# Optimization experiments

Measured on AMD Instinct MI355X. Metric: run time of the kernel, lower is better.

Reference implementation:

```python
import jax, jax.numpy as jnp
import numpy as np

NEG_SLOPE = 0.2


def setup_inputs() -> dict:
    key = jax.random.key(0)
    k1, k2, k3, k4, k5 = jax.random.split(key, 5)
    N, F_in, F_out, H, D = 4096, 256, 256, 4, 64
    x = jax.random.normal(k1, (N, F_in), dtype=jnp.float32)
    adj = jax.random.normal(k2, (N, N), dtype=jnp.float32)  # ~half entries > 0 -> edges
    W = jax.random.normal(k3, (F_out, F_in), dtype=jnp.float32) * (1.0 / np.sqrt(F_in))
    a_src = jax.random.normal(k4, (H, D), dtype=jnp.float32) * 0.1
    a_dst = jax.random.normal(k5, (H, D), dtype=jnp.float32) * 0.1
    return {"x": x, "adj": adj, "W": W, "a_src": a_src, "a_dst": a_dst}


def reference(x, adj, W, a_src, a_dst):
    N = x.shape[0]
    H, D = a_src.shape
    # linear projection (torch Linear: x @ W.T), reshape to heads
    h = (x @ W.T).reshape(N, H, D)                      # [N, H, D]
    attn_src = jnp.einsum('nhd,hd->nh', h, a_src)       # [N, H]
    attn_dst = jnp.einsum('nhd,hd->nh', h, a_dst)       # [N, H]
    scores = attn_src[:, None, :] + attn_dst[None, :, :]  # [N, N, H]
    scores = jnp.where(scores >= 0, scores, NEG_SLOPE * scores)  # leaky_relu(0.2)
    mask = (adj > 0)[:, :, None]                        # [N, N, 1]
    scores = jnp.where(mask, scores, -jnp.inf)
    attn = jax.nn.softmax(scores, axis=1)               # softmax over neighbors j
    attn = jnp.nan_to_num(attn, nan=0.0)                # fully-masked rows -> 0
    weighted = attn * adj[:, :, None]                   # weight by adjacency values
    out = jnp.einsum('ijh,jhd->ihd', weighted, h)       # [N, H, D]
    return out.reshape(N, H * D)
```

## Files before the change

### kernel.cpp

```cpp
#include <hip/hip_runtime.h>
#include <stdint.h>

#define NN 4096
#define FF 256
#define HH 4
#define DD 64
#define NEG 0.2f
#define LOG2E 1.4426950408889634f

#define ITILE 32
#define CJ 64
#define NB (NN / 8)

typedef __attribute__((ext_vector_type(8))) short short8;
typedef __attribute__((ext_vector_type(4))) float f32x4;
typedef __attribute__((ext_vector_type(16))) float f32x16;

__device__ __forceinline__ uint16_t bf16_rh(float f) {
    uint32_t u = __float_as_uint(f);
    return (uint16_t)((u + 0x8000u) >> 16);
}
__device__ __forceinline__ uint32_t cvtpk(float lo, float hi) {
    uint32_t r;
    asm("v_cvt_pk_bf16_f32 %0, %1, %2" : "=v"(r) : "v"(lo), "v"(hi));
    return r;
}

__global__ __launch_bounds__(256) void gemm_h(const float* __restrict__ x,
                                              const float* __restrict__ W,
                                              const float* __restrict__ a_src,
                                              const float* __restrict__ a_dst,
                                              float* __restrict__ s,
                                              float* __restrict__ T_T,
                                              uint16_t* __restrict__ Bf,
                                              float* __restrict__ pden) {
    __shared__ uint16_t xs[64][264];
    __shared__ uint16_t wsl[64][264];
    const int tid = threadIdx.x;
    if (blockIdx.y == 0) pden[blockIdx.x * 256 + tid] = 0.f;
    const int i0g = blockIdx.x * 64;
    const int f0 = blockIdx.y * 64;
    const int hh = blockIdx.y;
    const float* xsrc = x + (size_t)i0g * FF;
    const float* wsrc = W + (size_t)f0 * FF;
    {
        const int rw = tid >> 6, c4 = (tid & 63) * 4;
#pragma unroll
        for (int p = 0; p < 16; p++) {
            float4 vx = ((const float4*)xsrc)[p * 256 + tid];
            float4 vw = ((const float4*)wsrc)[p * 256 + tid];
            *(uint2*)&xs[p * 4 + rw][c4] =
                make_uint2(cvtpk(vx.x, vx.y), cvtpk(vx.z, vx.w));
            *(uint2*)&wsl[p * 4 + rw][c4] =
                make_uint2(cvtpk(vw.x, vw.y), cvtpk(vw.z, vw.w));
        }
    }
    __syncthreads();
    const int w = tid >> 6, l = tid & 63;
    const int m = l & 15, q = l >> 4;
    const int i0 = i0g + w * 16;
    f32x4 acc[4];
#pragma unroll
    for (int n = 0; n < 4; n++)
#pragma unroll
        for (int r = 0; r < 4; r++) acc[n][r] = 0.f;
    const uint16_t* ax = &xs[w * 16 + m][q * 8];
#pragma unroll
    for (int k0 = 0; k0 < 8; k0++) {
        short8 af = *(const short8*)(ax + k0 * 32);
#pragma unroll
        for (int n = 0; n < 4; n++) {
            short8 bf = *(const short8*)&wsl[n * 16 + m][k0 * 32 + q * 8];
            acc[n] = __builtin_amdgcn_mfma_f32_16x16x32_bf16(af, bf, acc[n], 0, 0, 0);
        }
    }
    const float* as = a_src + hh * DD;
    const float* ad = a_dst + hh * DD;
    float av[4], dv[4];
#pragma unroll
    for (int n = 0; n < 4; n++) { av[n] = as[n * 16 + m]; dv[n] = ad[n * 16 + m]; }
#pragma unroll
    for (int r = 0; r < 4; r++) {
        float vs = 0.f, vd = 0.f;
#pragma unroll
        for (int n = 0; n < 4; n++) {
            vs = fmaf(acc[n][r], av[n], vs);
            vd = fmaf(acc[n][r], dv[n], vd);
        }
#pragma unroll
        for (int off = 1; off < 16; off <<= 1) {
            vs += __shfl_xor(vs, off, 64);
            vd += __shfl_xor(vd, off, 64);
        }
        if (m == 0) {
            const int i = i0 + q * 4 + r;
            s[(size_t)i * HH + hh] = vs * LOG2E;
            T_T[(size_t)hh * NN + i] = vd * LOG2E;
        }
    }
    const int iblk = blockIdx.x * 8 + w * 2 + (q >> 1);
    const int jjo  = (q & 1) * 4;
#pragma unroll
    for (int n = 0; n < 4; n++) {
        *(uint2*)(Bf + (((size_t)hh * NB + iblk) * 64 + n * 16 + m) * 8 + jjo) =
            make_uint2(cvtpk(acc[n][0], acc[n][1]), cvtpk(acc[n][2], acc[n][3]));
    }
}

template<int NSt>
__global__ __launch_bounds__(256, 4) void gat_main(
    const float* __restrict__ adj, const uint16_t* __restrict__ Bf,
    const float* __restrict__ s, const float* __restrict__ T_T,
    float* __restrict__ pden, uint16_t* __restrict__ part) {
    constexpr int JRt = NN / NSt;
    constexpr int NCH = JRt / CJ;
    __shared__ float adj_s[2][CJ][32];
    __shared__ float ts[2][HH][CJ];
    const int tid = threadIdx.x;
    const int w = tid >> 6, l = tid & 63;
    const int m = l & 31, q = l >> 5;
    constexpr int NWG = (NN / ITILE) * NSt;
    const int orig = blockIdx.y * (NN / ITILE) + blockIdx.x;
    const int swz = (orig & 7) * (NWG / 8) + (orig >> 3);
    const int i0 = (swz & (NN / ITILE - 1)) * ITILE;
    const int sl = swz / (NN / ITILE);
    const int jb = sl * JRt;

    const float sS = s[(size_t)(i0 + m) * HH + w];
    const float sB = NEG * sS;
    float den = 0.f;
    f32x16 acc0, acc1;
#pragma unroll
    for (int r = 0; r < 16; r++) { acc0[r] = 0.f; acc1[r] = 0.f; }
    const uint16_t* bbase = Bf + (size_t)w * NB * 512;
    const float* tsrc = T_T + (size_t)w * NN + l;

    const int is = tid >> 3, r7 = tid & 7, j8 = r7 * 8;
    const int colw = is ^ (r7 << 2);
    const float* arow = adj + (size_t)(i0 + is) * NN + j8;

    float4 p0 = *(const float4*)(arow + jb);
    float4 p1 = *(const float4*)(arow + jb + 4);
    float tp = tsrc[jb];
    adj_s[0][j8 + 0][colw] = p0.x; adj_s[0][j8 + 1][colw] = p0.y;
    adj_s[0][j8 + 2][colw] = p0.z; adj_s[0][j8 + 3][colw] = p0.w;
    adj_s[0][j8 + 4][colw] = p1.x; adj_s[0][j8 + 5][colw] = p1.y;
    adj_s[0][j8 + 6][colw] = p1.z; adj_s[0][j8 + 7][colw] = p1.w;
    ts[0][w][l] = tp;
    p0 = *(const float4*)(arow + jb + CJ);
    p1 = *(const float4*)(arow + jb + CJ + 4);
    tp = tsrc[jb + CJ];
    __syncthreads();

    for (int c = 0; c < NCH; ++c) {
        const int jc = jb + c * CJ;
        const int cur = c & 1;
        if (c + 1 < NCH) {
            const int nb = cur ^ 1;
            adj_s[nb][j8 + 0][colw] = p0.x; adj_s[nb][j8 + 1][colw] = p0.y;
            adj_s[nb][j8 + 2][colw] = p0.z; adj_s[nb][j8 + 3][colw] = p0.w;
            adj_s[nb][j8 + 4][colw] = p1.x; adj_s[nb][j8 + 5][colw] = p1.y;
            adj_s[nb][j8 + 6][colw] = p1.z; adj_s[nb][j8 + 7][colw] = p1.w;
            ts[nb][w][l] = tp;
            if (c + 2 < NCH) {
                p0 = *(const float4*)(arow + jc + 2 * CJ);
                p1 = *(const float4*)(arow + jc + 2 * CJ + 4);
                tp = tsrc[jc + 2 * CJ];
            }
        }
#pragma unroll
        for (int kk = 0; kk < CJ; kk += 16) {
            const int jblk = ((jc + kk) >> 3) + q;
            const int cmv = m ^ ((((kk >> 3) + q) & 7) << 2);
            const float* tptr = &ts[cur][w][kk + q * 8];
            float4 t0 = *(const float4*)tptr;
            float4 t1 = *(const float4*)(tptr + 4);
            short8 bf0 = *(const short8*)(bbase + (size_t)jblk * 512 + m * 8);
            short8 bf1 = *(const short8*)(bbase + (size_t)jblk * 512 + (32 + m) * 8);
            float tt[8] = {t0.x, t0.y, t0.z, t0.w, t1.x, t1.y, t1.z, t1.w};
            union { uint32_t u[4]; short8 v; } afu;
#pragma unroll
            for (int jj = 0; jj < 8; jj += 2) {
                const int rr = kk + q * 8 + jj;
                float a0 = adj_s[cur][rr][cmv], a1 = adj_s[cur][rr + 1][cmv];
                float tv0 = tt[jj], tv1 = tt[jj + 1];
                float x0 = sS + tv0,           x1 = sS + tv1;
                float z0 = fmaf(NEG, tv0, sB), z1 = fmaf(NEG, tv1, sB);
                float lr0 = fmaxf(x0, z0), lr1 = fmaxf(x1, z1);
                float e0, e1;
                asm("v_exp_f32 %0, %1" : "=v"(e0) : "v"(lr0));
                asm("v_exp_f32 %0, %1" : "=v"(e1) : "v"(lr1));
                e0 = (a0 > 0.f) ? e0 : 0.f;
                e1 = (a1 > 0.f) ? e1 : 0.f;
                den += e0 + e1;
                afu.u[jj >> 1] = cvtpk(e0 * a0, e1 * a1);
            }
            acc0 = __builtin_amdgcn_mfma_f32_32x32x16_bf16(afu.v, bf0, acc0, 0, 0, 0);
            acc1 = __builtin_amdgcn_mfma_f32_32x32x16_bf16(afu.v, bf1, acc1, 0, 0, 0);
        }
        __syncthreads();
    }
    den += __shfl_down(den, 32, 64);
    if (l < 32) atomicAdd(&pden[(size_t)(i0 + m) * HH + w], den);
    uint16_t* pbase = part + (size_t)sl * NN * FF;
#pragma unroll
    for (int reg = 0; reg < 16; reg++) {
        int row = (reg & 3) + 8 * (reg >> 2) + 4 * q;
        pbase[(size_t)(i0 + row) * FF + w * DD + m]      = bf16_rh(acc0[reg]);
        pbase[(size_t)(i0 + row) * FF + w * DD + 32 + m] = bf16_rh(acc1[reg]);
    }
}

template<int NSt>
__global__ __launch_bounds__(256) void finalize(const uint16_t* __restrict__ part,
                                                const float* __restrict__ pden,
                                                float* __restrict__ out) {
    const int i = blockIdx.x * 8 + (threadIdx.x >> 5);
    const int f8 = (threadIdx.x & 31) * 8;
    float acc[8];
#pragma unroll
    for (int e = 0; e < 8; e++) acc[e] = 0.f;
#pragma unroll
    for (int sl = 0; sl < NSt; sl++) {
        union { short8 v; uint16_t u[8]; } b;
        b.v = *(const short8*)(part + (size_t)sl * NN * FF + (size_t)i * FF + f8);
#pragma unroll
        for (int e = 0; e < 8; e++)
            acc[e] += __uint_as_float(((uint32_t)b.u[e]) << 16);
    }
    float d = pden[(size_t)i * HH + (f8 >> 6)];
    float inv = (d > 0.f) ? 1.f / d : 0.f;
    *(float4*)(out + (size_t)i * FF + f8) =
        make_float4(acc[0] * inv, acc[1] * inv, acc[2] * inv, acc[3] * inv);
    *(float4*)(out + (size_t)i * FF + f8 + 4) =
        make_float4(acc[4] * inv, acc[5] * inv, acc[6] * inv, acc[7] * inv);
}

extern "C" void kernel_launch(void* const* d_in, const int* in_sizes, int n_in,
                              void* d_out, int out_size, void* d_ws, size_t ws_size,
                              hipStream_t stream) {
    const float* x     = (const float*)d_in[0];
    const float* adj   = (const float*)d_in[1];
    const float* W     = (const float*)d_in[2];
    const float* a_src = (const float*)d_in[3];
    const float* a_dst = (const float*)d_in[4];
    float* out = (float*)d_out;

    char* ws = (char*)d_ws;
    uint16_t* Bf   = (uint16_t*)ws;
    float*    s    = (float*)(ws + (2u << 20));
    float*    T_T  = s + (size_t)NN * HH;
    float*    pden = T_T + (size_t)HH * NN;
    uint16_t* part = (uint16_t*)(ws + (3u << 20));

    gemm_h<<<dim3(NN / 64, HH), 256, 0, stream>>>(x, W, a_src, a_dst, s, T_T, Bf, pden);
    if (ws_size >= (3u << 20) + (size_t)16 * NN * FF * sizeof(uint16_t)) {
        gat_main<16><<<dim3(NN / ITILE, 16), 256, 0, stream>>>(adj, Bf, s, T_T, pden, part);
        finalize<16><<<NN / 8, 256, 0, stream>>>(part, pden, out);
    } else {
        gat_main<8><<<dim3(NN / ITILE, 8), 256, 0, stream>>>(adj, Bf, s, T_T, pden, part);
        finalize<8><<<NN / 8, 256, 0, stream>>>(part, pden, out);
    }
}
```

Baseline: 133.1 us.

## Use row-major padded adj tile, smaller gemm blocks, fixed 8-way j split

The adjacency tile in shared memory is now stored row-major with padding, replacing the XOR-swizzled transposed layout. This lets each lane read its 8 adjacency values with two float4 loads instead of eight scalar LDS reads, and stores become two float4 writes. The projection GEMM now uses 32-row, 128-thread blocks, doubling the grid for better CU occupancy. The j dimension is always split 8 ways instead of 16 when workspace allows, which halves partial-sum traffic but gives fewer workgroups and longer loops per block.

```diff
diff --git a/kernel.cpp b/kernel.cpp
--- a/kernel.cpp
+++ b/kernel.cpp
@@ -9,7 +9,10 @@
 #define LOG2E 1.4426950408889634f
 
 #define ITILE 32
+#define NS 8
+#define JR (NN / NS)
 #define CJ 64
+#define NCH (JR / CJ)
 #define NB (NN / 8)
 
 typedef __attribute__((ext_vector_type(8))) short short8;
@@ -26,7 +29,7 @@
     return r;
 }
 
-__global__ __launch_bounds__(256) void gemm_h(const float* __restrict__ x,
+__global__ __launch_bounds__(128) void gemm_h(const float* __restrict__ x,
                                               const float* __restrict__ W,
                                               const float* __restrict__ a_src,
                                               const float* __restrict__ a_dst,
@@ -34,26 +37,28 @@
                                               float* __restrict__ T_T,
                                               uint16_t* __restrict__ Bf,
                                               float* __restrict__ pden) {
-    __shared__ uint16_t xs[64][264];
+    __shared__ uint16_t xs[32][264];
     __shared__ uint16_t wsl[64][264];
     const int tid = threadIdx.x;
-    if (blockIdx.y == 0) pden[blockIdx.x * 256 + tid] = 0.f;
-    const int i0g = blockIdx.x * 64;
+    if (blockIdx.y == 0) pden[blockIdx.x * 128 + tid] = 0.f;
+    const int i0g = blockIdx.x * 32;
     const int f0 = blockIdx.y * 64;
     const int hh = blockIdx.y;
     const float* xsrc = x + (size_t)i0g * FF;
     const float* wsrc = W + (size_t)f0 * FF;
-    {
-        const int rw = tid >> 6, c4 = (tid & 63) * 4;
-#pragma unroll
-        for (int p = 0; p < 16; p++) {
-            float4 vx = ((const float4*)xsrc)[p * 256 + tid];
-            float4 vw = ((const float4*)wsrc)[p * 256 + tid];
-            *(uint2*)&xs[p * 4 + rw][c4] =
-                make_uint2(cvtpk(vx.x, vx.y), cvtpk(vx.z, vx.w));
-            *(uint2*)&wsl[p * 4 + rw][c4] =
-                make_uint2(cvtpk(vw.x, vw.y), cvtpk(vw.z, vw.w));
-        }
+#pragma unroll
+    for (int p = 0; p < 16; p++) {
+        const int gi = p * 128 + tid;
+        float4 vx = ((const float4*)xsrc)[gi];
+        *(uint2*)&xs[gi >> 6][(gi & 63) * 4] =
+            make_uint2(cvtpk(vx.x, vx.y), cvtpk(vx.z, vx.w));
+    }
+#pragma unroll
+    for (int p = 0; p < 32; p++) {
+        const int gi = p * 128 + tid;
+        float4 vw = ((const float4*)wsrc)[gi];
+        *(uint2*)&wsl[gi >> 6][(gi & 63) * 4] =
+            make_uint2(cvtpk(vw.x, vw.y), cvtpk(vw.z, vw.w));
     }
     __syncthreads();
     const int w = tid >> 6, l = tid & 63;
@@ -98,7 +103,7 @@
             T_T[(size_t)hh * NN + i] = vd * LOG2E;
         }
     }
-    const int iblk = blockIdx.x * 8 + w * 2 + (q >> 1);
+    const int iblk = blockIdx.x * 4 + w * 2 + (q >> 1);
     const int jjo  = (q & 1) * 4;
 #pragma unroll
     for (int n = 0; n < 4; n++) {
@@ -107,24 +112,21 @@
     }
 }
 
-template<int NSt>
 __global__ __launch_bounds__(256, 4) void gat_main(
     const float* __restrict__ adj, const uint16_t* __restrict__ Bf,
     const float* __restrict__ s, const float* __restrict__ T_T,
     float* __restrict__ pden, uint16_t* __restrict__ part) {
-    constexpr int JRt = NN / NSt;
-    constexpr int NCH = JRt / CJ;
-    __shared__ float adj_s[2][CJ][32];
+    __shared__ float adj_t[2][32][68];
     __shared__ float ts[2][HH][CJ];
     const int tid = threadIdx.x;
     const int w = tid >> 6, l = tid & 63;
     const int m = l & 31, q = l >> 5;
-    constexpr int NWG = (NN / ITILE) * NSt;
+    constexpr int NWG = (NN / ITILE) * NS;
     const int orig = blockIdx.y * (NN / ITILE) + blockIdx.x;
     const int swz = (orig & 7) * (NWG / 8) + (orig >> 3);
     const int i0 = (swz & (NN / ITILE - 1)) * ITILE;
     const int sl = swz / (NN / ITILE);
-    const int jb = sl * JRt;
+    const int jb = sl * JR;
 
     const float sS = s[(size_t)(i0 + m) * HH + w];
     const float sB = NEG * sS;
@@ -136,16 +138,13 @@
     const float* tsrc = T_T + (size_t)w * NN + l;
 
     const int is = tid >> 3, r7 = tid & 7, j8 = r7 * 8;
-    const int colw = is ^ (r7 << 2);
     const float* arow = adj + (size_t)(i0 + is) * NN + j8;
 
     float4 p0 = *(const float4*)(arow + jb);
     float4 p1 = *(const float4*)(arow + jb + 4);
     float tp = tsrc[jb];
-    adj_s[0][j8 + 0][colw] = p0.x; adj_s[0][j8 + 1][colw] = p0.y;
-    adj_s[0][j8 + 2][colw] = p0.z; adj_s[0][j8 + 3][colw] = p0.w;
-    adj_s[0][j8 + 4][colw] = p1.x; adj_s[0][j8 + 5][colw] = p1.y;
-    adj_s[0][j8 + 6][colw] = p1.z; adj_s[0][j8 + 7][colw] = p1.w;
+    *(float4*)&adj_t[0][is][j8]     = p0;
+    *(float4*)&adj_t[0][is][j8 + 4] = p1;
     ts[0][w][l] = tp;
     p0 = *(const float4*)(arow + jb + CJ);
     p1 = *(const float4*)(arow + jb + CJ + 4);
@@ -157,10 +156,8 @@
         const int cur = c & 1;
         if (c + 1 < NCH) {
             const int nb = cur ^ 1;
-            adj_s[nb][j8 + 0][colw] = p0.x; adj_s[nb][j8 + 1][colw] = p0.y;
-            adj_s[nb][j8 + 2][colw] = p0.z; adj_s[nb][j8 + 3][colw] = p0.w;
-            adj_s[nb][j8 + 4][colw] = p1.x; adj_s[nb][j8 + 5][colw] = p1.y;
-            adj_s[nb][j8 + 6][colw] = p1.z; adj_s[nb][j8 + 7][colw] = p1.w;
+            *(float4*)&adj_t[nb][is][j8]     = p0;
+            *(float4*)&adj_t[nb][is][j8 + 4] = p1;
             ts[nb][w][l] = tp;
             if (c + 2 < NCH) {
                 p0 = *(const float4*)(arow + jc + 2 * CJ);
@@ -171,18 +168,20 @@
 #pragma unroll
         for (int kk = 0; kk < CJ; kk += 16) {
             const int jblk = ((jc + kk) >> 3) + q;
-            const int cmv = m ^ ((((kk >> 3) + q) & 7) << 2);
+            const float* ap = &adj_t[cur][m][kk + q * 8];
+            float4 a0v = *(const float4*)ap;
+            float4 a1v = *(const float4*)(ap + 4);
             const float* tptr = &ts[cur][w][kk + q * 8];
             float4 t0 = *(const float4*)tptr;
             float4 t1 = *(const float4*)(tptr + 4);
             short8 bf0 = *(const short8*)(bbase + (size_t)jblk * 512 + m * 8);
             short8 bf1 = *(const short8*)(bbase + (size_t)jblk * 512 + (32 + m) * 8);
+            float aa[8] = {a0v.x, a0v.y, a0v.z, a0v.w, a1v.x, a1v.y, a1v.z, a1v.w};
             float tt[8] = {t0.x, t0.y, t0.z, t0.w, t1.x, t1.y, t1.z, t1.w};
             union { uint32_t u[4]; short8 v; } afu;
 #pragma unroll
             for (int jj = 0; jj < 8; jj += 2) {
-                const int rr = kk + q * 8 + jj;
-                float a0 = adj_s[cur][rr][cmv], a1 = adj_s[cur][rr + 1][cmv];
+                float a0 = aa[jj], a1 = aa[jj + 1];
                 float tv0 = tt[jj], tv1 = tt[jj + 1];
                 float x0 = sS + tv0,           x1 = sS + tv1;
                 float z0 = fmaf(NEG, tv0, sB), z1 = fmaf(NEG, tv1, sB);
@@ -211,7 +210,6 @@
     }
 }
 
-template<int NSt>
 __global__ __launch_bounds__(256) void finalize(const uint16_t* __restrict__ part,
                                                 const float* __restrict__ pden,
                                                 float* __restrict__ out) {
@@ -221,7 +219,7 @@
 #pragma unroll
     for (int e = 0; e < 8; e++) acc[e] = 0.f;
 #pragma unroll
-    for (int sl = 0; sl < NSt; sl++) {
+    for (int sl = 0; sl < NS; sl++) {
         union { short8 v; uint16_t u[8]; } b;
         b.v = *(const short8*)(part + (size_t)sl * NN * FF + (size_t)i * FF + f8);
 #pragma unroll
@@ -253,12 +251,7 @@
     float*    pden = T_T + (size_t)HH * NN;
     uint16_t* part = (uint16_t*)(ws + (3u << 20));
 
-    gemm_h<<<dim3(NN / 64, HH), 256, 0, stream>>>(x, W, a_src, a_dst, s, T_T, Bf, pden);
-    if (ws_size >= (3u << 20) + (size_t)16 * NN * FF * sizeof(uint16_t)) {
-        gat_main<16><<<dim3(NN / ITILE, 16), 256, 0, stream>>>(adj, Bf, s, T_T, pden, part);
-        finalize<16><<<NN / 8, 256, 0, stream>>>(part, pden, out);
-    } else {
-        gat_main<8><<<dim3(NN / ITILE, 8), 256, 0, stream>>>(adj, Bf, s, T_T, pden, part);
-        finalize<8><<<NN / 8, 256, 0, stream>>>(part, pden, out);
-    }
-}
+    gemm_h<<<dim3(NN / 32, HH), 128, 0, stream>>>(x, W, a_src, a_dst, s, T_T, Bf, pden);
+    gat_main<<<dim3(NN / ITILE, NS), 256, 0, stream>>>(adj, Bf, s, T_T, pden, part);
+    finalize<<<NN / 8, 256, 0, stream>>>(part, pden, out);
+}
```

After: 130.9 us. Within noise of the previous version (-1.7%).
